# Kernel optimization log

Measured on AMD Instinct MI355X. Metric: run time of the kernel, lower is better.

## Reference

```python
import jax, jax.numpy as jnp
import numpy as np

B, S, I, H, C = 512, 512, 28, 128, 10


def setup_inputs() -> dict:
    key = jax.random.key(0)
    ks = jax.random.split(key, 11)
    std = 1.0 / np.sqrt(H)  # torch nn.RNN init scale
    u = lambda k, shape: jax.random.uniform(k, shape, jnp.float32, -std, std)
    return {
        "x": jax.random.normal(ks[0], (B, S, I), jnp.float32),
        "W_ih0": u(ks[1], (H, I)),
        "W_hh0": u(ks[2], (H, H)),
        "b_ih0": u(ks[3], (H,)),
        "b_hh0": u(ks[4], (H,)),
        "W_ih1": u(ks[5], (H, H)),
        "W_hh1": u(ks[6], (H, H)),
        "b_ih1": u(ks[7], (H,)),
        "b_hh1": u(ks[8], (H,)),
        "W_fc": u(ks[9], (C, H)),
        "b_fc": u(ks[10], (C,)),
    }


def reference(x, W_ih0, W_hh0, b_ih0, b_hh0, W_ih1, W_hh1, b_ih1, b_hh1, W_fc, b_fc):
    # 2-layer tanh RNN (batch_first); only the last timestep of layer 1 feeds fc,
    # so we carry hidden states through a scan without storing outputs.
    b = x.shape[0]
    h0_init = jnp.zeros((b, W_hh0.shape[0]), x.dtype)
    h1_init = jnp.zeros((b, W_hh1.shape[0]), x.dtype)

    def step(carry, xt):  # xt: [B, I]
        h0, h1 = carry
        h0 = jnp.tanh(xt @ W_ih0.T + b_ih0 + h0 @ W_hh0.T + b_hh0)
        h1 = jnp.tanh(h0 @ W_ih1.T + b_ih1 + h1 @ W_hh1.T + b_hh1)
        return (h0, h1), None

    xs = jnp.swapaxes(x, 0, 1)  # [S, B, I] time-major for scan
    (h0, h1), _ = jax.lax.scan(step, (h0_init, h1_init), xs)
    return h1 @ W_fc.T + b_fc  # [B, C]
```

## Files before the change

kernel.cpp:

```cpp
#include <hip/hip_runtime.h>

#define SEQ   512
#define IN    28
#define HID   128
#define NCLS  10
#define MB    16
#define PCH   160
#define MAGICF 12582912.0f

typedef __attribute__((ext_vector_type(4))) int   i32x4;
typedef __attribute__((ext_vector_type(4))) float f32x4;
typedef __attribute__((ext_vector_type(8))) short short8v;

#define SH_AA (1.0f/130048.0f)

__device__ __forceinline__ unsigned short f2bf(float f) {
    unsigned u = __float_as_uint(f);
    return (unsigned short)((u + 0x7FFFu + ((u >> 16) & 1u)) >> 16);
}
__device__ __forceinline__ unsigned cvtpk(float a, float b) {
    unsigned r;
    asm("v_cvt_pk_bf16_f32 %0, %1, %2" : "=v"(r) : "v"(a), "v"(b));
    return r;
}
__device__ __forceinline__ float fast_tanh(float x) {
    float e = exp2f(x * 2.8853900817779268f);
    return 1.0f - 2.0f * __builtin_amdgcn_rcpf(e + 1.0f);
}
__device__ __forceinline__ f32x4 mfma_bf(short8v a, short8v b, f32x4 c) {
    return __builtin_amdgcn_mfma_f32_16x16x32_bf16(a, b, c, 0, 0, 0);
}
__device__ __forceinline__ i32x4 mfma_i8(i32x4 a, i32x4 b, i32x4 c) {
    return __builtin_amdgcn_mfma_i32_16x16x64_i8(a, b, c, 0, 0, 0);
}
__device__ __forceinline__ void quantW(float wv, signed char& qa, signed char& qb) {
    int a = (int)rintf(wv * 1024.0f);
    float r = fmaf((float)a, -1.0f / 1024.0f, wv);
    int b = (int)rintf(r * 262144.0f);
    b = b > 127 ? 127 : (b < -127 ? -127 : b);
    qa = (signed char)a;
    qb = (signed char)b;
}
__device__ __forceinline__ unsigned quant4a(float t0, float t1, float t2, float t3) {
    unsigned u0 = __float_as_uint(fmaf(t0, 127.0f, MAGICF));
    unsigned u1 = __float_as_uint(fmaf(t1, 127.0f, MAGICF));
    unsigned u2 = __float_as_uint(fmaf(t2, 127.0f, MAGICF));
    unsigned u3 = __float_as_uint(fmaf(t3, 127.0f, MAGICF));
    unsigned t01 = __builtin_amdgcn_perm(u1, u0, 0x00000400u);
    unsigned t23 = __builtin_amdgcn_perm(u3, u2, 0x00000400u);
    return __builtin_amdgcn_perm(t23, t01, 0x05040100u);
}

union FragI8 { i32x4 v; signed char c[16]; };
union FragBF { short8v s; unsigned u[4]; };

__global__ __launch_bounds__(1024)
void rnn2_i8u(const float* __restrict__ x,
              const float* __restrict__ W_ih0, const float* __restrict__ W_hh0,
              const float* __restrict__ b_ih0, const float* __restrict__ b_hh0,
              const float* __restrict__ W_ih1, const float* __restrict__ W_hh1,
              const float* __restrict__ b_ih1, const float* __restrict__ b_hh1,
              const float* __restrict__ W_fc,  const float* __restrict__ b_fc,
              float* __restrict__ out)
{
    __shared__ __attribute__((aligned(16))) signed char hmem[2][2][MB * PCH];
    __shared__ float hfin[MB][HID + 4];

    const int t    = threadIdx.x;
    const int lane = t & 63;
    const int w    = t >> 6;
    const int lm   = lane & 15;
    const int lg   = lane >> 4;
    const int b0   = blockIdx.x * MB;
    const bool isL0 = (w < 8);
    const int T    = isL0 ? w : (w - 8);
    const int j    = 16 * T + lm;

    i32x4 Wa[2][2], Wb[2][2];
    short8v WxH = {};
    float biasv[4];

    if (isL0) {
        #pragma unroll
        for (int kt = 0; kt < 2; ++kt) {
            const float* p = W_hh0 + j * HID + 64 * kt + 16 * lg;
            FragI8 a, b;
            #pragma unroll
            for (int e = 0; e < 16; ++e) quantW(p[e], a.c[e], b.c[e]);
            Wa[0][kt] = a.v; Wb[0][kt] = b.v;
        }
        FragBF H;
        #pragma unroll
        for (int p = 0; p < 4; ++p) {
            const int k0 = 8 * lg + 2 * p, k1 = k0 + 1;
            float w0 = (k0 < IN) ? W_ih0[j * IN + k0] : 0.0f;
            float w1 = (k1 < IN) ? W_ih0[j * IN + k1] : 0.0f;
            H.u[p] = (unsigned)f2bf(w0) | ((unsigned)f2bf(w1) << 16);
        }
        WxH = H.s;
        #pragma unroll
        for (int r = 0; r < 4; ++r) {
            const int u = 16 * T + 4 * lg + r;
            biasv[r] = b_ih0[u] + b_hh0[u];
        }
    } else {
        #pragma unroll
        for (int kt = 0; kt < 2; ++kt) {
            const float* p1 = W_ih1 + j * HID + 64 * kt + 16 * lg;
            const float* p2 = W_hh1 + j * HID + 64 * kt + 16 * lg;
            FragI8 a1, q1, a2, q2;
            #pragma unroll
            for (int e = 0; e < 16; ++e) {
                quantW(p1[e], a1.c[e], q1.c[e]);
                quantW(p2[e], a2.c[e], q2.c[e]);
            }
            Wa[0][kt] = a1.v; Wb[0][kt] = q1.v;
            Wa[1][kt] = a2.v; Wb[1][kt] = q2.v;
        }
        #pragma unroll
        for (int r = 0; r < 4; ++r) {
            const int u = 16 * T + 4 * lg + r;
            biasv[r] = b_ih1[u] + b_hh1[u];
        }
    }

    {
        int* z = (int*)&hmem[0][0][0];
        #pragma unroll
        for (int i = 0; i < 3; ++i) {
            const int idx = t + i * 1024;
            if (idx < (int)(sizeof(hmem) / 4)) z[idx] = 0;
        }
    }

    const float* xp = x + ((size_t)(b0 + lm) * SEQ) * IN + 8 * lg;
    float4 xA = make_float4(0.f, 0.f, 0.f, 0.f), xB = xA;
    if (isL0) {
        xA = *(const float4*)xp;
        if (lg < 3) xB = *(const float4*)(xp + 4);
    }
    __syncthreads();

    const int rbase = lm * PCH + 16 * lg;
    const int wbase = lm * PCH + 16 * T + 4 * lg;
    const i32x4 z4 = {0, 0, 0, 0};

    if (isL0) {
        FragBF H;
        H.u[0] = cvtpk(xA.x, xA.y);
        H.u[1] = cvtpk(xA.z, xA.w);
        H.u[2] = cvtpk(xB.x, xB.y);
        H.u[3] = cvtpk(xB.z, xB.w);
        {
            const float* p = xp + IN;
            xA = *(const float4*)p;
            xB = (lg < 3) ? *(const float4*)(p + 4) : make_float4(0.f, 0.f, 0.f, 0.f);
        }
        f32x4 accx = {biasv[0], biasv[1], biasv[2], biasv[3]};
        accx = mfma_bf(WxH, H.s, accx);
        *(unsigned*)&hmem[0][1][wbase] = quant4a(fast_tanh(accx[0]), fast_tanh(accx[1]),
                                                 fast_tanh(accx[2]), fast_tanh(accx[3]));
    }
    __syncthreads();

    for (int it = 1; it < SEQ; ++it) {
        const int rd = it & 1, wr = rd ^ 1;

        if (isL0) {
            i32x4 Ba0[2];
            Ba0[0] = *(const i32x4*)&hmem[0][rd][rbase];
            Ba0[1] = *(const i32x4*)&hmem[0][rd][rbase + 64];

            FragBF H;
            H.u[0] = cvtpk(xA.x, xA.y);
            H.u[1] = cvtpk(xA.z, xA.w);
            H.u[2] = cvtpk(xB.x, xB.y);
            H.u[3] = cvtpk(xB.z, xB.w);
            {
                const int tn = (it < SEQ - 1) ? it + 1 : it;
                const float* p = xp + (size_t)tn * IN;
                xA = *(const float4*)p;
                xB = (lg < 3) ? *(const float4*)(p + 4) : make_float4(0.f, 0.f, 0.f, 0.f);
            }

            f32x4 accx = {biasv[0], biasv[1], biasv[2], biasv[3]};
            accx = mfma_bf(WxH, H.s, accx);

            i32x4 aa = mfma_i8(Wa[0][0], Ba0[0], z4);
            aa = mfma_i8(Wa[0][1], Ba0[1], aa);
            i32x4 cr = mfma_i8(Wb[0][0], Ba0[0], z4);
            cr = mfma_i8(Wb[0][1], Ba0[1], cr);

            float t0 = fast_tanh(fmaf(SH_AA, fmaf((float)cr[0], 1.0f / 256.0f, (float)aa[0]), accx[0]));
            float t1 = fast_tanh(fmaf(SH_AA, fmaf((float)cr[1], 1.0f / 256.0f, (float)aa[1]), accx[1]));
            float t2 = fast_tanh(fmaf(SH_AA, fmaf((float)cr[2], 1.0f / 256.0f, (float)aa[2]), accx[2]));
            float t3 = fast_tanh(fmaf(SH_AA, fmaf((float)cr[3], 1.0f / 256.0f, (float)aa[3]), accx[3]));
            *(unsigned*)&hmem[0][wr][wbase] = quant4a(t0, t1, t2, t3);
        } else {
            i32x4 Ba0[2], Ba1[2];
            Ba0[0] = *(const i32x4*)&hmem[0][rd][rbase];
            Ba0[1] = *(const i32x4*)&hmem[0][rd][rbase + 64];
            Ba1[0] = *(const i32x4*)&hmem[1][rd][rbase];
            Ba1[1] = *(const i32x4*)&hmem[1][rd][rbase + 64];

            i32x4 aa = mfma_i8(Wa[0][0], Ba0[0], z4);
            aa = mfma_i8(Wa[0][1], Ba0[1], aa);
            aa = mfma_i8(Wa[1][0], Ba1[0], aa);
            aa = mfma_i8(Wa[1][1], Ba1[1], aa);
            i32x4 cr = mfma_i8(Wb[0][0], Ba0[0], z4);
            cr = mfma_i8(Wb[0][1], Ba0[1], cr);
            cr = mfma_i8(Wb[1][0], Ba1[0], cr);
            cr = mfma_i8(Wb[1][1], Ba1[1], cr);

            float t0 = fast_tanh(fmaf(SH_AA, fmaf((float)cr[0], 1.0f / 256.0f, (float)aa[0]), biasv[0]));
            float t1 = fast_tanh(fmaf(SH_AA, fmaf((float)cr[1], 1.0f / 256.0f, (float)aa[1]), biasv[1]));
            float t2 = fast_tanh(fmaf(SH_AA, fmaf((float)cr[2], 1.0f / 256.0f, (float)aa[2]), biasv[2]));
            float t3 = fast_tanh(fmaf(SH_AA, fmaf((float)cr[3], 1.0f / 256.0f, (float)aa[3]), biasv[3]));
            *(unsigned*)&hmem[1][wr][wbase] = quant4a(t0, t1, t2, t3);
        }
        __syncthreads();
    }

    if (!isL0) {
        i32x4 Ba0[2], Ba1[2];
        Ba0[0] = *(const i32x4*)&hmem[0][0][rbase];
        Ba0[1] = *(const i32x4*)&hmem[0][0][rbase + 64];
        Ba1[0] = *(const i32x4*)&hmem[1][0][rbase];
        Ba1[1] = *(const i32x4*)&hmem[1][0][rbase + 64];

        i32x4 aa = mfma_i8(Wa[0][0], Ba0[0], z4);
        aa = mfma_i8(Wa[0][1], Ba0[1], aa);
        aa = mfma_i8(Wa[1][0], Ba1[0], aa);
        aa = mfma_i8(Wa[1][1], Ba1[1], aa);
        i32x4 cr = mfma_i8(Wb[0][0], Ba0[0], z4);
        cr = mfma_i8(Wb[0][1], Ba0[1], cr);
        cr = mfma_i8(Wb[1][0], Ba1[0], cr);
        cr = mfma_i8(Wb[1][1], Ba1[1], cr);

        const int u = 16 * T + 4 * lg;
        hfin[lm][u + 0] = fast_tanh(fmaf(SH_AA, fmaf((float)cr[0], 1.0f / 256.0f, (float)aa[0]), biasv[0]));
        hfin[lm][u + 1] = fast_tanh(fmaf(SH_AA, fmaf((float)cr[1], 1.0f / 256.0f, (float)aa[1]), biasv[1]));
        hfin[lm][u + 2] = fast_tanh(fmaf(SH_AA, fmaf((float)cr[2], 1.0f / 256.0f, (float)aa[2]), biasv[2]));
        hfin[lm][u + 3] = fast_tanh(fmaf(SH_AA, fmaf((float)cr[3], 1.0f / 256.0f, (float)aa[3]), biasv[3]));
    }
    __syncthreads();

    if (t < MB * NCLS) {
        const int r = t / NCLS, c = t % NCLS;
        float acc = b_fc[c];
        const float* hf = &hfin[r][0];
        #pragma unroll 4
        for (int k = 0; k < HID; ++k)
            acc = fmaf(W_fc[c * HID + k], hf[k], acc);
        out[(b0 + r) * NCLS + c] = acc;
    }
}

extern "C" void kernel_launch(void* const* d_in, const int* in_sizes, int n_in,
                              void* d_out, int out_size, void* d_ws, size_t ws_size,
                              hipStream_t stream) {
    const float* x     = (const float*)d_in[0];
    const float* W_ih0 = (const float*)d_in[1];
    const float* W_hh0 = (const float*)d_in[2];
    const float* b_ih0 = (const float*)d_in[3];
    const float* b_hh0 = (const float*)d_in[4];
    const float* W_ih1 = (const float*)d_in[5];
    const float* W_hh1 = (const float*)d_in[6];
    const float* b_ih1 = (const float*)d_in[7];
    const float* b_hh1 = (const float*)d_in[8];
    const float* W_fc  = (const float*)d_in[9];
    const float* b_fc  = (const float*)d_in[10];
    float* out = (float*)d_out;

    rnn2_i8u<<<dim3(512 / MB), dim3(1024), 0, stream>>>(
        x, W_ih0, W_hh0, b_ih0, b_hh0, W_ih1, W_hh1, b_ih1, b_hh1, W_fc, b_fc, out);
}
```

Before: 353.2 us.

## Pre-convert x to padded bf16 in workspace and merge int8 split dequant

Adds a separate pre-pass kernel that converts x to bf16 rows padded to 32 elements in the workspace. The recurrent kernel can then load one 16-byte fragment per step instead of two float4 loads plus four pack conversions. It also folds the hi/lo int8 partial sums into one integer ((aa<<8)+cr) before a single float convert and FMA, which removes one convert and one FMA per element on the serial path. The cost is an extra kernel launch and a full read/write pass over x, plus a fallback when the workspace is too small. The combined integer could overflow precision in float for large sums.

```diff
diff --git a/kernel.cpp b/kernel.cpp
--- a/kernel.cpp
+++ b/kernel.cpp
@@ -6,13 +6,14 @@
 #define NCLS  10
 #define MB    16
 #define PCH   160
+#define XPCH  32
 #define MAGICF 12582912.0f
 
 typedef __attribute__((ext_vector_type(4))) int   i32x4;
 typedef __attribute__((ext_vector_type(4))) float f32x4;
 typedef __attribute__((ext_vector_type(8))) short short8v;
 
-#define SH_AA (1.0f/130048.0f)
+#define SH_CR (1.0f/33292288.0f)
 
 __device__ __forceinline__ unsigned short f2bf(float f) {
     unsigned u = __float_as_uint(f);
@@ -54,8 +55,25 @@
 union FragI8 { i32x4 v; signed char c[16]; };
 union FragBF { short8v s; unsigned u[4]; };
 
+__global__ __launch_bounds__(256)
+void xconv(const float* __restrict__ x, unsigned short* __restrict__ xb)
+{
+    const int r = blockIdx.x * 256 + threadIdx.x;
+    const float* src = x + (size_t)r * IN;
+    unsigned d[16];
+    #pragma unroll
+    for (int p = 0; p < 14; ++p) d[p] = cvtpk(src[2 * p], src[2 * p + 1]);
+    d[14] = 0u; d[15] = 0u;
+    uint4* dst = (uint4*)(xb + (size_t)r * XPCH);
+    dst[0] = make_uint4(d[0], d[1], d[2], d[3]);
+    dst[1] = make_uint4(d[4], d[5], d[6], d[7]);
+    dst[2] = make_uint4(d[8], d[9], d[10], d[11]);
+    dst[3] = make_uint4(d[12], d[13], d[14], d[15]);
+}
+
+template<bool XPRE>
 __global__ __launch_bounds__(1024)
-void rnn2_i8u(const float* __restrict__ x,
+void rnn2_i8v(const float* __restrict__ x, const unsigned short* __restrict__ xb,
               const float* __restrict__ W_ih0, const float* __restrict__ W_hh0,
               const float* __restrict__ b_ih0, const float* __restrict__ b_hh0,
               const float* __restrict__ W_ih1, const float* __restrict__ W_hh1,
@@ -133,11 +151,17 @@
         }
     }
 
-    const float* xp = x + ((size_t)(b0 + lm) * SEQ) * IN + 8 * lg;
+    const unsigned short* xrow = xb + ((size_t)(b0 + lm) * SEQ) * XPCH + 8 * lg;
+    const float* xpf = x + ((size_t)(b0 + lm) * SEQ) * IN + 8 * lg;
+    short8v Xn = {};
     float4 xA = make_float4(0.f, 0.f, 0.f, 0.f), xB = xA;
     if (isL0) {
-        xA = *(const float4*)xp;
-        if (lg < 3) xB = *(const float4*)(xp + 4);
+        if constexpr (XPRE) {
+            Xn = *(const short8v*)xrow;
+        } else {
+            xA = *(const float4*)xpf;
+            if (lg < 3) xB = *(const float4*)(xpf + 4);
+        }
     }
     __syncthreads();
 
@@ -146,55 +170,66 @@
     const i32x4 z4 = {0, 0, 0, 0};
 
     if (isL0) {
-        FragBF H;
-        H.u[0] = cvtpk(xA.x, xA.y);
-        H.u[1] = cvtpk(xA.z, xA.w);
-        H.u[2] = cvtpk(xB.x, xB.y);
-        H.u[3] = cvtpk(xB.z, xB.w);
-        {
-            const float* p = xp + IN;
-            xA = *(const float4*)p;
-            xB = (lg < 3) ? *(const float4*)(p + 4) : make_float4(0.f, 0.f, 0.f, 0.f);
-        }
-        f32x4 accx = {biasv[0], biasv[1], biasv[2], biasv[3]};
-        accx = mfma_bf(WxH, H.s, accx);
-        *(unsigned*)&hmem[0][1][wbase] = quant4a(fast_tanh(accx[0]), fast_tanh(accx[1]),
-                                                 fast_tanh(accx[2]), fast_tanh(accx[3]));
-    }
-    __syncthreads();
-
-    for (int it = 1; it < SEQ; ++it) {
-        const int rd = it & 1, wr = rd ^ 1;
-
-        if (isL0) {
-            i32x4 Ba0[2];
-            Ba0[0] = *(const i32x4*)&hmem[0][rd][rbase];
-            Ba0[1] = *(const i32x4*)&hmem[0][rd][rbase + 64];
-
+        short8v Xc;
+        if constexpr (XPRE) {
+            Xc = Xn;
+            Xn = *(const short8v*)(xrow + XPCH);
+        } else {
             FragBF H;
             H.u[0] = cvtpk(xA.x, xA.y);
             H.u[1] = cvtpk(xA.z, xA.w);
             H.u[2] = cvtpk(xB.x, xB.y);
             H.u[3] = cvtpk(xB.z, xB.w);
-            {
+            Xc = H.s;
+            const float* p = xpf + IN;
+            xA = *(const float4*)p;
+            xB = (lg < 3) ? *(const float4*)(p + 4) : make_float4(0.f, 0.f, 0.f, 0.f);
+        }
+        f32x4 accx = {biasv[0], biasv[1], biasv[2], biasv[3]};
+        accx = mfma_bf(WxH, Xc, accx);
+        *(unsigned*)&hmem[0][1][wbase] = quant4a(fast_tanh(accx[0]), fast_tanh(accx[1]),
+                                                 fast_tanh(accx[2]), fast_tanh(accx[3]));
+    }
+    __syncthreads();
+
+    for (int it = 1; it < SEQ; ++it) {
+        const int rd = it & 1, wr = rd ^ 1;
+
+        if (isL0) {
+            i32x4 Ba0[2];
+            Ba0[0] = *(const i32x4*)&hmem[0][rd][rbase];
+            Ba0[1] = *(const i32x4*)&hmem[0][rd][rbase + 64];
+
+            short8v Xc;
+            if constexpr (XPRE) {
+                Xc = Xn;
                 const int tn = (it < SEQ - 1) ? it + 1 : it;
-                const float* p = xp + (size_t)tn * IN;
+                Xn = *(const short8v*)(xrow + (size_t)tn * XPCH);
+            } else {
+                FragBF H;
+                H.u[0] = cvtpk(xA.x, xA.y);
+                H.u[1] = cvtpk(xA.z, xA.w);
+                H.u[2] = cvtpk(xB.x, xB.y);
+                H.u[3] = cvtpk(xB.z, xB.w);
+                Xc = H.s;
+                const int tn = (it < SEQ - 1) ? it + 1 : it;
+                const float* p = xpf + (size_t)tn * IN;
                 xA = *(const float4*)p;
                 xB = (lg < 3) ? *(const float4*)(p + 4) : make_float4(0.f, 0.f, 0.f, 0.f);
             }
 
             f32x4 accx = {biasv[0], biasv[1], biasv[2], biasv[3]};
-            accx = mfma_bf(WxH, H.s, accx);
+            accx = mfma_bf(WxH, Xc, accx);
 
             i32x4 aa = mfma_i8(Wa[0][0], Ba0[0], z4);
             aa = mfma_i8(Wa[0][1], Ba0[1], aa);
             i32x4 cr = mfma_i8(Wb[0][0], Ba0[0], z4);
             cr = mfma_i8(Wb[0][1], Ba0[1], cr);
 
-            float t0 = fast_tanh(fmaf(SH_AA, fmaf((float)cr[0], 1.0f / 256.0f, (float)aa[0]), accx[0]));
-            float t1 = fast_tanh(fmaf(SH_AA, fmaf((float)cr[1], 1.0f / 256.0f, (float)aa[1]), accx[1]));
-            float t2 = fast_tanh(fmaf(SH_AA, fmaf((float)cr[2], 1.0f / 256.0f, (float)aa[2]), accx[2]));
-            float t3 = fast_tanh(fmaf(SH_AA, fmaf((float)cr[3], 1.0f / 256.0f, (float)aa[3]), accx[3]));
+            float t0 = fast_tanh(fmaf((float)((aa[0] << 8) + cr[0]), SH_CR, accx[0]));
+            float t1 = fast_tanh(fmaf((float)((aa[1] << 8) + cr[1]), SH_CR, accx[1]));
+            float t2 = fast_tanh(fmaf((float)((aa[2] << 8) + cr[2]), SH_CR, accx[2]));
+            float t3 = fast_tanh(fmaf((float)((aa[3] << 8) + cr[3]), SH_CR, accx[3]));
             *(unsigned*)&hmem[0][wr][wbase] = quant4a(t0, t1, t2, t3);
         } else {
             i32x4 Ba0[2], Ba1[2];
@@ -212,10 +247,10 @@
             cr = mfma_i8(Wb[1][0], Ba1[0], cr);
             cr = mfma_i8(Wb[1][1], Ba1[1], cr);
 
-            float t0 = fast_tanh(fmaf(SH_AA, fmaf((float)cr[0], 1.0f / 256.0f, (float)aa[0]), biasv[0]));
-            float t1 = fast_tanh(fmaf(SH_AA, fmaf((float)cr[1], 1.0f / 256.0f, (float)aa[1]), biasv[1]));
-            float t2 = fast_tanh(fmaf(SH_AA, fmaf((float)cr[2], 1.0f / 256.0f, (float)aa[2]), biasv[2]));
-            float t3 = fast_tanh(fmaf(SH_AA, fmaf((float)cr[3], 1.0f / 256.0f, (float)aa[3]), biasv[3]));
+            float t0 = fast_tanh(fmaf((float)((aa[0] << 8) + cr[0]), SH_CR, biasv[0]));
+            float t1 = fast_tanh(fmaf((float)((aa[1] << 8) + cr[1]), SH_CR, biasv[1]));
+            float t2 = fast_tanh(fmaf((float)((aa[2] << 8) + cr[2]), SH_CR, biasv[2]));
+            float t3 = fast_tanh(fmaf((float)((aa[3] << 8) + cr[3]), SH_CR, biasv[3]));
             *(unsigned*)&hmem[1][wr][wbase] = quant4a(t0, t1, t2, t3);
         }
         __syncthreads();
@@ -238,10 +273,10 @@
         cr = mfma_i8(Wb[1][1], Ba1[1], cr);
 
         const int u = 16 * T + 4 * lg;
-        hfin[lm][u + 0] = fast_tanh(fmaf(SH_AA, fmaf((float)cr[0], 1.0f / 256.0f, (float)aa[0]), biasv[0]));
-        hfin[lm][u + 1] = fast_tanh(fmaf(SH_AA, fmaf((float)cr[1], 1.0f / 256.0f, (float)aa[1]), biasv[1]));
-        hfin[lm][u + 2] = fast_tanh(fmaf(SH_AA, fmaf((float)cr[2], 1.0f / 256.0f, (float)aa[2]), biasv[2]));
-        hfin[lm][u + 3] = fast_tanh(fmaf(SH_AA, fmaf((float)cr[3], 1.0f / 256.0f, (float)aa[3]), biasv[3]));
+        hfin[lm][u + 0] = fast_tanh(fmaf((float)((aa[0] << 8) + cr[0]), SH_CR, biasv[0]));
+        hfin[lm][u + 1] = fast_tanh(fmaf((float)((aa[1] << 8) + cr[1]), SH_CR, biasv[1]));
+        hfin[lm][u + 2] = fast_tanh(fmaf((float)((aa[2] << 8) + cr[2]), SH_CR, biasv[2]));
+        hfin[lm][u + 3] = fast_tanh(fmaf((float)((aa[3] << 8) + cr[3]), SH_CR, biasv[3]));
     }
     __syncthreads();
 
@@ -272,6 +307,16 @@
     const float* b_fc  = (const float*)d_in[10];
     float* out = (float*)d_out;
 
-    rnn2_i8u<<<dim3(512 / MB), dim3(1024), 0, stream>>>(
-        x, W_ih0, W_hh0, b_ih0, b_hh0, W_ih1, W_hh1, b_ih1, b_hh1, W_fc, b_fc, out);
-}
+    const size_t xb_bytes = (size_t)512 * SEQ * XPCH * sizeof(unsigned short);
+    if (ws_size >= xb_bytes) {
+        unsigned short* xbuf = (unsigned short*)d_ws;
+        xconv<<<dim3(512 * SEQ / 256), dim3(256), 0, stream>>>(x, xbuf);
+        rnn2_i8v<true><<<dim3(512 / MB), dim3(1024), 0, stream>>>(
+            x, xbuf, W_ih0, W_hh0, b_ih0, b_hh0, W_ih1, W_hh1, b_ih1, b_hh1,
+            W_fc, b_fc, out);
+    } else {
+        rnn2_i8v<false><<<dim3(512 / MB), dim3(1024), 0, stream>>>(
+            x, nullptr, W_ih0, W_hh0, b_ih0, b_hh0, W_ih1, W_hh1, b_ih1, b_hh1,
+            W_fc, b_fc, out);
+    }
+}
```

After: 361.5 us. +2.3%, slower.
